# Performance work log

Hardware: AMD Instinct MI355X
Metric: run time of the kernel (lower is better)

Reference implementation:

```python
import jax, jax.numpy as jnp
import numpy as np

L, B, S, D = 12, 2, 2048, 768
QK, H, V = 128, 512, 32000
SCALE = 128 ** (-0.5)


def setup_inputs() -> dict:
    key = jax.random.key(0)
    ks = jax.random.split(key, 11)
    p = lambda k, shp: jax.random.normal(k, shp, dtype=jnp.float32) * 0.02
    return {
        "layer_outputs": jax.random.normal(ks[0], (L, B, S, D), dtype=jnp.float32),
        "Wq": p(ks[1], (D, QK)), "bq": jnp.zeros((QK,), jnp.float32),
        "Wk": p(ks[2], (D, QK)), "bk": jnp.zeros((QK,), jnp.float32),
        "Wv": p(ks[3], (D, H)),  "bv": jnp.zeros((H,), jnp.float32),
        "W1": p(ks[4], (H, H // 2)), "b1": jnp.zeros((H // 2,), jnp.float32),
        "W2": p(ks[5], (H // 2, V)), "b2": jnp.zeros((V,), jnp.float32),
    }


def reference(layer_outputs, Wq, bq, Wk, bk, Wv, bv, W1, b1, W2, b2):
    # layer_outputs: (L, B, S, D) -> h: (S, L, B, D) as in torch permute(2,0,1,3)
    h = jnp.transpose(layer_outputs, (2, 0, 1, 3))
    q_in = h.mean(axis=1)                              # (S, B, D)
    q = jax.nn.relu(q_in @ Wq + bq)                    # (S, B, 128)
    k = jax.nn.relu(h @ Wk + bk)                       # (S, L, B, 128)
    scores = jnp.einsum('sbd,slbd->slb', q, k)[..., None] * SCALE  # (S, L, B, 1)
    attn = jax.nn.softmax(scores, axis=1)              # softmax over layer axis
    v = h @ Wv + bv                                    # (S, L, B, H)
    agg = jnp.sum(attn * v, axis=1)                    # (S, B, H)
    agg = jnp.transpose(agg, (1, 0, 2))                # (B, S, H)
    mid = jax.nn.relu(agg @ W1 + b1)                   # (B, S, H//2); dropout is eval-mode identity
    return mid @ W2 + b2                               # (B, S, V)
```

## Files before the change

kernel.cpp:

```cpp
#include <hip/hip_runtime.h>

#define Snum 2048
#define SCALE 0.08838834764831845f

typedef __attribute__((ext_vector_type(8))) __bf16 bf16x8;
typedef __attribute__((ext_vector_type(4))) float f32x4;

__device__ inline unsigned short f2bf(float f) {
    unsigned int u = __float_as_uint(f);
    unsigned int r = u + 0x7FFFu + ((u >> 16) & 1u);
    return (unsigned short)(r >> 16);
}
__device__ inline float bf2f(unsigned short u) {
    return __uint_as_float(((unsigned)u) << 16);
}
__device__ inline void gld_lds16(const unsigned short* g, unsigned short* l) {
    __builtin_amdgcn_global_load_lds(
        (const __attribute__((address_space(1))) unsigned int*)g,
        (__attribute__((address_space(3))) unsigned int*)l, 16, 0, 0);
}

__global__ __launch_bounds__(256) void prep_weights(
    const float* __restrict__ Wv, unsigned short* __restrict__ Wvbf,
    const float* __restrict__ W1, unsigned short* __restrict__ W1t,
    const float* __restrict__ Wk, const float* __restrict__ Wq,
    unsigned short* __restrict__ Wqkt)
{
    const int id = blockIdx.x;
    if (id < 384) {
        const int base = (id * 256 + threadIdx.x) * 4;
        const float4 v = *(const float4*)(Wv + base);
        ushort4 o;
        o.x = f2bf(v.x); o.y = f2bf(v.y); o.z = f2bf(v.z); o.w = f2bf(v.w);
        *(ushort4*)(Wvbf + base) = o;
        return;
    }
    __shared__ float t[32][33];
    const float* in; unsigned short* out; int K, N, bx, by;
    if (id < 512)      { int q = id - 384; in = W1; out = W1t;  K = 512; N = 256; bx = q & 7; by = q >> 3; }
    else if (id < 608) { int q = id - 512; in = Wk; out = Wqkt; K = 768; N = 128; bx = q & 3; by = q >> 2; }
    else               { int q = id - 608; in = Wq; out = Wqkt + (size_t)128 * 768; K = 768; N = 128; bx = q & 3; by = q >> 2; }

    const int tx = threadIdx.x & 31, ty = threadIdx.x >> 5;
    #pragma unroll
    for (int i = 0; i < 4; ++i) {
        int k = by * 32 + ty + i * 8, n = bx * 32 + tx;
        t[ty + i * 8][tx] = in[(size_t)k * N + n];
    }
    __syncthreads();
    #pragma unroll
    for (int i = 0; i < 4; ++i) {
        int n = bx * 32 + ty + i * 8, k = by * 32 + tx;
        out[(size_t)n * K + k] = f2bf(t[tx][ty + i * 8]);
    }
}

__global__ __launch_bounds__(256) void bias_prime(
    const unsigned short* __restrict__ W1t, const float* __restrict__ bv,
    const float* __restrict__ b1, float* __restrict__ bp)
{
    const int n = threadIdx.x;
    float s = b1[n];
    const unsigned short* row = W1t + (size_t)n * 512;
    for (int h = 0; h < 512; h += 8) {
        uint4 u = *(const uint4*)(row + h);
        const unsigned short* v = (const unsigned short*)&u;
        #pragma unroll
        for (int i = 0; i < 8; ++i) s += bv[h + i] * bf2f(v[i]);
    }
    bp[n] = s;
}

__global__ __launch_bounds__(256) void proj_qk(
    const float* __restrict__ x, const unsigned short* __restrict__ Bt,
    const float* __restrict__ bk,
    unsigned short* __restrict__ Kall,
    unsigned short* __restrict__ Pq)
{
    __shared__ __align__(16) unsigned short As[2][64 * 32];
    __shared__ __align__(16) unsigned short Bs[2][256 * 32];
    const int tid = threadIdx.x;
    const int wid = tid >> 6, lane = tid & 63;
    const int wn = wid * 64;
    const int lr = lane & 15, g = lane >> 4;
    const int r0 = blockIdx.x * 64;
    const int K = 768, NT = 24;

    const int arow = tid >> 2, akc = (tid & 3) * 8;

    f32x4 acc[4][4] = {};

    float4 a0 = *(const float4*)(x + (size_t)(r0 + arow) * K + akc);
    float4 a1 = *(const float4*)(x + (size_t)(r0 + arow) * K + akc + 4);
    {
        unsigned short v[8];
        v[0] = f2bf(a0.x); v[1] = f2bf(a0.y); v[2] = f2bf(a0.z); v[3] = f2bf(a0.w);
        v[4] = f2bf(a1.x); v[5] = f2bf(a1.y); v[6] = f2bf(a1.z); v[7] = f2bf(a1.w);
        *(uint4*)&As[0][arow * 32 + akc] = *(uint4*)v;
    }
    #pragma unroll
    for (int c = 0; c < 4; ++c) {
        const int rr = wid * 64 + c * 16;
        gld_lds16(Bt + (size_t)(rr + (lane >> 2)) * K + (lane & 3) * 8, &Bs[0][rr * 32]);
    }
    __syncthreads();

    for (int t = 0; t < NT; ++t) {
        const int cur = t & 1, nxt = cur ^ 1;
        if (t + 1 < NT) {
            const int k0 = (t + 1) * 32;
            a0 = *(const float4*)(x + (size_t)(r0 + arow) * K + k0 + akc);
            a1 = *(const float4*)(x + (size_t)(r0 + arow) * K + k0 + akc + 4);
            #pragma unroll
            for (int c = 0; c < 4; ++c) {
                const int rr = wid * 64 + c * 16;
                gld_lds16(Bt + (size_t)(rr + (lane >> 2)) * K + k0 + (lane & 3) * 8,
                          &Bs[nxt][rr * 32]);
            }
        }

        bf16x8 aF[4], bF[4];
        #pragma unroll
        for (int mm = 0; mm < 4; ++mm) aF[mm] = *(const bf16x8*)&As[cur][(mm * 16 + lr) * 32 + g * 8];
        #pragma unroll
        for (int nn = 0; nn < 4; ++nn) bF[nn] = *(const bf16x8*)&Bs[cur][(wn + nn * 16 + lr) * 32 + g * 8];
        #pragma unroll
        for (int mm = 0; mm < 4; ++mm)
            #pragma unroll
            for (int nn = 0; nn < 4; ++nn)
                acc[mm][nn] = __builtin_amdgcn_mfma_f32_16x16x32_bf16(bF[nn], aF[mm], acc[mm][nn], 0, 0, 0);

        if (t + 1 < NT) {
            unsigned short v[8];
            v[0] = f2bf(a0.x); v[1] = f2bf(a0.y); v[2] = f2bf(a0.z); v[3] = f2bf(a0.w);
            v[4] = f2bf(a1.x); v[5] = f2bf(a1.y); v[6] = f2bf(a1.z); v[7] = f2bf(a1.w);
            *(uint4*)&As[nxt][arow * 32 + akc] = *(uint4*)v;
        }
        __syncthreads();
    }

    #pragma unroll
    for (int mm = 0; mm < 4; ++mm)
        #pragma unroll
        for (int nn = 0; nn < 4; ++nn) {
            const int row = r0 + mm * 16 + lr;
            const int colb = wn + nn * 16 + g * 4;
            unsigned short o[4];
            if (colb < 128) {
                #pragma unroll
                for (int reg = 0; reg < 4; ++reg) {
                    float kv = acc[mm][nn][reg] + bk[colb + reg];
                    o[reg] = f2bf(kv > 0.f ? kv : 0.f);
                }
                *(ushort4*)&Kall[(size_t)row * 128 + colb] = *(ushort4*)o;
            } else {
                #pragma unroll
                for (int reg = 0; reg < 4; ++reg) o[reg] = f2bf(acc[mm][nn][reg]);
                *(ushort4*)&Pq[(size_t)row * 128 + (colb - 128)] = *(ushort4*)o;
            }
        }
}

__global__ __launch_bounds__(256) void scores_plus_w2t(
    const float* __restrict__ x,
    const unsigned short* __restrict__ Pq,
    const float* __restrict__ bq,
    const unsigned short* __restrict__ Kall,
    unsigned short* __restrict__ hbar,
    const float* __restrict__ W2, unsigned short* __restrict__ W2t)
{
    if (blockIdx.x >= 1024) {
        __shared__ float t[32][33];
        const int id = blockIdx.x - 1024;
        const int bx = id >> 3, by = id & 7;
        const int tx = threadIdx.x & 31, ty = threadIdx.x >> 5;
        #pragma unroll
        for (int i = 0; i < 4; ++i) {
            int k = by * 32 + ty + i * 8, n = bx * 32 + tx;
            t[ty + i * 8][tx] = W2[(size_t)k * 32000 + n];
        }
        __syncthreads();
        #pragma unroll
        for (int i = 0; i < 4; ++i) {
            int n = bx * 32 + ty + i * 8, k = by * 32 + tx;
            W2t[(size_t)n * 256 + k] = f2bf(t[tx][ty + i * 8]);
        }
        return;
    }

    const int wid = threadIdx.x >> 6, lane = threadIdx.x & 63;
    const int r = blockIdx.x * 4 + wid;
    const int b = r >> 11, s = r & 2047;

    float qa = 0.f, qb_ = 0.f;
    #pragma unroll
    for (int l = 0; l < 12; ++l) {
        const unsigned short* prow = Pq + ((size_t)(l * 2 + b) * Snum + s) * 128 + lane * 2;
        unsigned int u = *(const unsigned int*)prow;
        qa += bf2f((unsigned short)(u & 0xFFFF));
        qb_ += bf2f((unsigned short)(u >> 16));
    }
    float q0 = qa * (1.0f / 12.0f) + bq[lane * 2];
    float q1 = qb_ * (1.0f / 12.0f) + bq[lane * 2 + 1];
    q0 = q0 > 0.f ? q0 : 0.f;
    q1 = q1 > 0.f ? q1 : 0.f;
    q0 = bf2f(f2bf(q0)); q1 = bf2f(f2bf(q1));

    float sc[12];
    #pragma unroll
    for (int l = 0; l < 12; ++l) {
        const unsigned short* krow = Kall + ((size_t)(l * 2 + b) * Snum + s) * 128 + lane * 2;
        unsigned int u = *(const unsigned int*)krow;
        float p = q0 * bf2f((unsigned short)(u & 0xFFFF)) + q1 * bf2f((unsigned short)(u >> 16));
        #pragma unroll
        for (int off = 32; off > 0; off >>= 1) p += __shfl_xor(p, off, 64);
        sc[l] = p * SCALE;
    }
    float m = sc[0];
    #pragma unroll
    for (int l = 1; l < 12; ++l) m = fmaxf(m, sc[l]);
    float att[12], den = 0.f;
    #pragma unroll
    for (int l = 0; l < 12; ++l) { att[l] = __expf(sc[l] - m); den += att[l]; }
    const float inv = 1.0f / den;
    #pragma unroll
    for (int l = 0; l < 12; ++l) att[l] *= inv;

    #pragma unroll
    for (int jv = 0; jv < 3; ++jv) {
        const int d0 = jv * 256 + lane * 4;
        float a0 = 0.f, a1 = 0.f, a2 = 0.f, a3 = 0.f;
        #pragma unroll
        for (int l = 0; l < 12; ++l) {
            const float4 v = *(const float4*)(x + ((size_t)(l * 2 + b) * Snum + s) * 768 + d0);
            a0 += att[l] * v.x; a1 += att[l] * v.y; a2 += att[l] * v.z; a3 += att[l] * v.w;
        }
        ushort4 o;
        o.x = f2bf(a0); o.y = f2bf(a1); o.z = f2bf(a2); o.w = f2bf(a3);
        *(ushort4*)(hbar + (size_t)r * 768 + d0) = o;
    }
}

template <int RELU, int OUT_BF16, int BIAS>
__global__ __launch_bounds__(256) void gemm64(
    const unsigned short* __restrict__ A, const unsigned short* __restrict__ Bt,
    const float* __restrict__ bias, void* __restrict__ out, int M, int N, int K)
{
    __shared__ __align__(16) unsigned short As[2][64 * 32];
    __shared__ __align__(16) unsigned short Bs[2][64 * 32];
    const int tid = threadIdx.x;
    const int bn = blockIdx.x, bm = blockIdx.y;
    const int wid = tid >> 6, lane = tid & 63;
    const int wm = (wid >> 1) * 32, wn = (wid & 1) * 32;
    const int lr = lane & 15, g = lane >> 4;
    const int r0 = bm * 64, c0 = bn * 64;
    const int NT = K / 32;

    const int srow = lane >> 2, skc = (lane & 3) * 8;

    f32x4 acc[2][2] = {};

    gld_lds16(A  + (size_t)(r0 + wid * 16 + srow) * K + skc, &As[0][wid * 16 * 32]);
    gld_lds16(Bt + (size_t)(c0 + wid * 16 + srow) * K + skc, &Bs[0][wid * 16 * 32]);
    __syncthreads();

    for (int t = 0; t < NT; ++t) {
        const int cur = t & 1, nxt = cur ^ 1;
        if (t + 1 < NT) {
            const int k0 = (t + 1) * 32;
            gld_lds16(A  + (size_t)(r0 + wid * 16 + srow) * K + k0 + skc, &As[nxt][wid * 16 * 32]);
            gld_lds16(Bt + (size_t)(c0 + wid * 16 + srow) * K + k0 + skc, &Bs[nxt][wid * 16 * 32]);
        }

        bf16x8 aF[2], bF[2];
        #pragma unroll
        for (int mm = 0; mm < 2; ++mm) aF[mm] = *(const bf16x8*)&As[cur][(wm + mm * 16 + lr) * 32 + g * 8];
        #pragma unroll
        for (int nn = 0; nn < 2; ++nn) bF[nn] = *(const bf16x8*)&Bs[cur][(wn + nn * 16 + lr) * 32 + g * 8];
        #pragma unroll
        for (int mm = 0; mm < 2; ++mm)
            #pragma unroll
            for (int nn = 0; nn < 2; ++nn)
                acc[mm][nn] = __builtin_amdgcn_mfma_f32_16x16x32_bf16(bF[nn], aF[mm], acc[mm][nn], 0, 0, 0);
        __syncthreads();
    }

    #pragma unroll
    for (int mm = 0; mm < 2; ++mm)
        #pragma unroll
        for (int nn = 0; nn < 2; ++nn) {
            const int orow = r0 + wm + mm * 16 + lr;
            const int colb = c0 + wn + nn * 16 + g * 4;
            float vr[4];
            #pragma unroll
            for (int reg = 0; reg < 4; ++reg) {
                float v = acc[mm][nn][reg] + (BIAS ? bias[colb + reg] : 0.f);
                vr[reg] = (RELU && v < 0.f) ? 0.f : v;
            }
            if (OUT_BF16) {
                unsigned short o[4];
                #pragma unroll
                for (int reg = 0; reg < 4; ++reg) o[reg] = f2bf(vr[reg]);
                *(ushort4*)&((unsigned short*)out)[(size_t)orow * N + colb] = *(ushort4*)o;
            } else {
                *(float4*)&((float*)out)[(size_t)orow * N + colb] = *(float4*)vr;
            }
        }
}

__global__ __launch_bounds__(256) void gemm_out(
    const unsigned short* __restrict__ A,
    const unsigned short* __restrict__ Bt,
    const float* __restrict__ bias, float* __restrict__ out)
{
    __shared__ __align__(16) unsigned short As[2][128 * 32];
    __shared__ __align__(16) unsigned short Bs[2][128 * 32];
    const int K = 256, N = 32000, NT = 8;
    const int orig = blockIdx.x;
    const int swz = (orig & 7) * 1000 + (orig >> 3);
    const int bn = swz >> 5, bm = swz & 31;
    const int tid = threadIdx.x;
    const int wid = tid >> 6, lane = tid & 63;
    const int wm = (wid >> 1) * 64, wn = (wid & 1) * 64;
    const int lr = lane & 15, g = lane >> 4;
    const int r0 = bm * 128, c0 = bn * 128;

    f32x4 acc[4][4] = {};

    #pragma unroll
    for (int c = 0; c < 2; ++c) {
        const int rr = wid * 32 + c * 16;
        gld_lds16(A  + (size_t)(r0 + rr + (lane >> 2)) * K + (lane & 3) * 8, &As[0][rr * 32]);
        gld_lds16(Bt + (size_t)(c0 + rr + (lane >> 2)) * K + (lane & 3) * 8, &Bs[0][rr * 32]);
    }
    __syncthreads();

    for (int t = 0; t < NT; ++t) {
        const int cur = t & 1, nxt = cur ^ 1;
        if (t + 1 < NT) {
            const int k0 = (t + 1) * 32;
            #pragma unroll
            for (int c = 0; c < 2; ++c) {
                const int rr = wid * 32 + c * 16;
                gld_lds16(A  + (size_t)(r0 + rr + (lane >> 2)) * K + k0 + (lane & 3) * 8, &As[nxt][rr * 32]);
                gld_lds16(Bt + (size_t)(c0 + rr + (lane >> 2)) * K + k0 + (lane & 3) * 8, &Bs[nxt][rr * 32]);
            }
        }

        bf16x8 aF[4], bF[4];
        #pragma unroll
        for (int mm = 0; mm < 4; ++mm) aF[mm] = *(const bf16x8*)&As[cur][(wm + mm * 16 + lr) * 32 + g * 8];
        #pragma unroll
        for (int nn = 0; nn < 4; ++nn) bF[nn] = *(const bf16x8*)&Bs[cur][(wn + nn * 16 + lr) * 32 + g * 8];
        #pragma unroll
        for (int mm = 0; mm < 4; ++mm)
            #pragma unroll
            for (int nn = 0; nn < 4; ++nn)
                acc[mm][nn] = __builtin_amdgcn_mfma_f32_16x16x32_bf16(bF[nn], aF[mm], acc[mm][nn], 0, 0, 0);
        __syncthreads();
    }

    #pragma unroll
    for (int mm = 0; mm < 4; ++mm)
        #pragma unroll
        for (int nn = 0; nn < 4; ++nn) {
            const int row = r0 + wm + mm * 16 + lr;
            const int colb = c0 + wn + nn * 16 + g * 4;
            const float4 b4 = *(const float4*)&bias[colb];
            f32x4 o = acc[mm][nn];
            o[0] += b4.x; o[1] += b4.y; o[2] += b4.z; o[3] += b4.w;
            __builtin_nontemporal_store(o, (f32x4*)&out[(size_t)row * N + colb]);
        }
}

extern "C" void kernel_launch(void* const* d_in, const int* in_sizes, int n_in,
                              void* d_out, int out_size, void* d_ws, size_t ws_size,
                              hipStream_t stream) {
    (void)in_sizes; (void)n_in; (void)out_size; (void)ws_size;

    const float* x  = (const float*)d_in[0];
    const float* Wq = (const float*)d_in[1];
    const float* bq = (const float*)d_in[2];
    const float* Wk = (const float*)d_in[3];
    const float* bk = (const float*)d_in[4];
    const float* Wv = (const float*)d_in[5];
    const float* bv = (const float*)d_in[6];
    const float* W1 = (const float*)d_in[7];
    const float* b1 = (const float*)d_in[8];
    const float* W2 = (const float*)d_in[9];
    const float* b2 = (const float*)d_in[10];

    char* p = (char*)d_ws;
    unsigned short* Wqkt  = (unsigned short*)p; p += (size_t)256 * 768 * 2;
    unsigned short* Wvbf  = (unsigned short*)p; p += (size_t)768 * 512 * 2;
    unsigned short* W1t   = (unsigned short*)p; p += (size_t)256 * 512 * 2;
    unsigned short* Gtb   = (unsigned short*)p; p += (size_t)256 * 768 * 2;
    float*          bprim = (float*)p;          p += (size_t)256 * 4;
    unsigned short* W2t   = (unsigned short*)p; p += (size_t)32000 * 256 * 2;
    unsigned short* Kall  = (unsigned short*)p; p += (size_t)49152 * 128 * 2;
    unsigned short* Pq    = (unsigned short*)p; p += (size_t)49152 * 128 * 2;
    unsigned short* hbar  = (unsigned short*)p; p += (size_t)4096 * 768 * 2;
    unsigned short* midb  = (unsigned short*)p; p += (size_t)4096 * 256 * 2;

    prep_weights<<<dim3(704), dim3(256), 0, stream>>>(Wv, Wvbf, W1, W1t, Wk, Wq, Wqkt);

    bias_prime<<<dim3(1), dim3(256), 0, stream>>>(W1t, bv, b1, bprim);

    gemm64<0, 1, 0><<<dim3(768 / 64, 256 / 64), dim3(256), 0, stream>>>(
        W1t, Wvbf, nullptr, Gtb, 256, 768, 512);

    proj_qk<<<dim3(49152 / 64), dim3(256), 0, stream>>>(x, Wqkt, bk, Kall, Pq);

    scores_plus_w2t<<<dim3(1024 + 8000), dim3(256), 0, stream>>>(
        x, Pq, bq, Kall, hbar, W2, W2t);

    gemm64<1, 1, 1><<<dim3(256 / 64, 4096 / 64), dim3(256), 0, stream>>>(
        hbar, Gtb, bprim, midb, 4096, 256, 768);

    gemm_out<<<dim3(8000), dim3(256), 0, stream>>>(midb, W2t, b2, (float*)d_out);
}
```

Baseline: 286.6 us.

## Use 32x32x16 MFMA in output GEMM and fuse bias-prime with G GEMM

The final vocabulary GEMM switches from 16x16x32 bf16 MFMAs to 32x32x16 MFMAs with 2x2 tiles per wave. This reduces the number of LDS fragment reads and MFMA issues per K step. Separately, the bias_prime kernel and the small W1t·Wv GEMM are merged into one 49-block launch, saving one kernel launch. The new output layout must map correctly to the 32x32 accumulator register ordering.

```diff
diff --git a/kernel.cpp b/kernel.cpp
--- a/kernel.cpp
+++ b/kernel.cpp
@@ -5,6 +5,7 @@
 
 typedef __attribute__((ext_vector_type(8))) __bf16 bf16x8;
 typedef __attribute__((ext_vector_type(4))) float f32x4;
+typedef __attribute__((ext_vector_type(16))) float f32x16;
 
 __device__ inline unsigned short f2bf(float f) {
     unsigned int u = __float_as_uint(f);
@@ -55,20 +56,74 @@
     }
 }
 
-__global__ __launch_bounds__(256) void bias_prime(
-    const unsigned short* __restrict__ W1t, const float* __restrict__ bv,
-    const float* __restrict__ b1, float* __restrict__ bp)
-{
-    const int n = threadIdx.x;
-    float s = b1[n];
-    const unsigned short* row = W1t + (size_t)n * 512;
-    for (int h = 0; h < 512; h += 8) {
-        uint4 u = *(const uint4*)(row + h);
-        const unsigned short* v = (const unsigned short*)&u;
-        #pragma unroll
-        for (int i = 0; i < 8; ++i) s += bv[h + i] * bf2f(v[i]);
-    }
-    bp[n] = s;
+__global__ __launch_bounds__(256) void gt_bias(
+    const unsigned short* __restrict__ W1t,
+    const unsigned short* __restrict__ Wvbf,
+    const float* __restrict__ bv, const float* __restrict__ b1,
+    unsigned short* __restrict__ Gtb,
+    float* __restrict__ bp)
+{
+    if (blockIdx.x == 48) {
+        const int n = threadIdx.x;
+        float s = b1[n];
+        const unsigned short* row = W1t + (size_t)n * 512;
+        for (int h = 0; h < 512; h += 8) {
+            uint4 u = *(const uint4*)(row + h);
+            const unsigned short* v = (const unsigned short*)&u;
+            #pragma unroll
+            for (int i = 0; i < 8; ++i) s += bv[h + i] * bf2f(v[i]);
+        }
+        bp[n] = s;
+        return;
+    }
+    __shared__ __align__(16) unsigned short As[2][64 * 32];
+    __shared__ __align__(16) unsigned short Bs[2][64 * 32];
+    const int tid = threadIdx.x;
+    const int bn = blockIdx.x % 12, bm = blockIdx.x / 12;
+    const int wid = tid >> 6, lane = tid & 63;
+    const int wm = (wid >> 1) * 32, wn = (wid & 1) * 32;
+    const int lr = lane & 15, g = lane >> 4;
+    const int r0 = bm * 64, c0 = bn * 64;
+    const int K = 512, NT = 16, N = 768;
+    const int srow = lane >> 2, skc = (lane & 3) * 8;
+
+    f32x4 acc[2][2] = {};
+
+    gld_lds16(W1t  + (size_t)(r0 + wid * 16 + srow) * K + skc, &As[0][wid * 16 * 32]);
+    gld_lds16(Wvbf + (size_t)(c0 + wid * 16 + srow) * K + skc, &Bs[0][wid * 16 * 32]);
+    __syncthreads();
+
+    for (int t = 0; t < NT; ++t) {
+        const int cur = t & 1, nxt = cur ^ 1;
+        if (t + 1 < NT) {
+            const int k0 = (t + 1) * 32;
+            gld_lds16(W1t  + (size_t)(r0 + wid * 16 + srow) * K + k0 + skc, &As[nxt][wid * 16 * 32]);
+            gld_lds16(Wvbf + (size_t)(c0 + wid * 16 + srow) * K + k0 + skc, &Bs[nxt][wid * 16 * 32]);
+        }
+        bf16x8 aF[2], bF[2];
+        #pragma unroll
+        for (int mm = 0; mm < 2; ++mm) aF[mm] = *(const bf16x8*)&As[cur][(wm + mm * 16 + lr) * 32 + g * 8];
+        #pragma unroll
+        for (int nn = 0; nn < 2; ++nn) bF[nn] = *(const bf16x8*)&Bs[cur][(wn + nn * 16 + lr) * 32 + g * 8];
+        #pragma unroll
+        for (int mm = 0; mm < 2; ++mm)
+            #pragma unroll
+            for (int nn = 0; nn < 2; ++nn)
+                acc[mm][nn] = __builtin_amdgcn_mfma_f32_16x16x32_bf16(bF[nn], aF[mm], acc[mm][nn], 0, 0, 0);
+        __syncthreads();
+    }
+
+    #pragma unroll
+    for (int mm = 0; mm < 2; ++mm)
+        #pragma unroll
+        for (int nn = 0; nn < 2; ++nn) {
+            const int orow = r0 + wm + mm * 16 + lr;
+            const int colb = c0 + wn + nn * 16 + g * 4;
+            unsigned short o[4];
+            #pragma unroll
+            for (int reg = 0; reg < 4; ++reg) o[reg] = f2bf(acc[mm][nn][reg]);
+            *(ushort4*)&Gtb[(size_t)orow * N + colb] = *(ushort4*)o;
+        }
 }
 
 __global__ __launch_bounds__(256) void proj_qk(
@@ -322,10 +377,10 @@
     const int tid = threadIdx.x;
     const int wid = tid >> 6, lane = tid & 63;
     const int wm = (wid >> 1) * 64, wn = (wid & 1) * 64;
-    const int lr = lane & 15, g = lane >> 4;
+    const int l31 = lane & 31, hi = lane >> 5;
     const int r0 = bm * 128, c0 = bn * 128;
 
-    f32x4 acc[4][4] = {};
+    f32x16 acc[2][2] = {};
 
     #pragma unroll
     for (int c = 0; c < 2; ++c) {
@@ -347,29 +402,40 @@
             }
         }
 
-        bf16x8 aF[4], bF[4];
-        #pragma unroll
-        for (int mm = 0; mm < 4; ++mm) aF[mm] = *(const bf16x8*)&As[cur][(wm + mm * 16 + lr) * 32 + g * 8];
-        #pragma unroll
-        for (int nn = 0; nn < 4; ++nn) bF[nn] = *(const bf16x8*)&Bs[cur][(wn + nn * 16 + lr) * 32 + g * 8];
-        #pragma unroll
-        for (int mm = 0; mm < 4; ++mm)
-            #pragma unroll
-            for (int nn = 0; nn < 4; ++nn)
-                acc[mm][nn] = __builtin_amdgcn_mfma_f32_16x16x32_bf16(bF[nn], aF[mm], acc[mm][nn], 0, 0, 0);
+        #pragma unroll
+        for (int ksub = 0; ksub < 2; ++ksub) {
+            bf16x8 aF[2], bF[2];
+            #pragma unroll
+            for (int mm = 0; mm < 2; ++mm)
+                aF[mm] = *(const bf16x8*)&As[cur][(wm + mm * 32 + l31) * 32 + ksub * 16 + hi * 8];
+            #pragma unroll
+            for (int nn = 0; nn < 2; ++nn)
+                bF[nn] = *(const bf16x8*)&Bs[cur][(wn + nn * 32 + l31) * 32 + ksub * 16 + hi * 8];
+            #pragma unroll
+            for (int mm = 0; mm < 2; ++mm)
+                #pragma unroll
+                for (int nn = 0; nn < 2; ++nn)
+                    acc[mm][nn] = __builtin_amdgcn_mfma_f32_32x32x16_bf16(bF[nn], aF[mm], acc[mm][nn], 0, 0, 0);
+        }
         __syncthreads();
     }
 
     #pragma unroll
-    for (int mm = 0; mm < 4; ++mm)
-        #pragma unroll
-        for (int nn = 0; nn < 4; ++nn) {
-            const int row = r0 + wm + mm * 16 + lr;
-            const int colb = c0 + wn + nn * 16 + g * 4;
-            const float4 b4 = *(const float4*)&bias[colb];
-            f32x4 o = acc[mm][nn];
-            o[0] += b4.x; o[1] += b4.y; o[2] += b4.z; o[3] += b4.w;
-            __builtin_nontemporal_store(o, (f32x4*)&out[(size_t)row * N + colb]);
+    for (int mm = 0; mm < 2; ++mm)
+        #pragma unroll
+        for (int nn = 0; nn < 2; ++nn) {
+            const int row = r0 + wm + mm * 32 + l31;
+            #pragma unroll
+            for (int q = 0; q < 4; ++q) {
+                const int colb = c0 + wn + nn * 32 + q * 8 + hi * 4;
+                const float4 b4 = *(const float4*)&bias[colb];
+                f32x4 o;
+                o[0] = acc[mm][nn][q * 4 + 0] + b4.x;
+                o[1] = acc[mm][nn][q * 4 + 1] + b4.y;
+                o[2] = acc[mm][nn][q * 4 + 2] + b4.z;
+                o[3] = acc[mm][nn][q * 4 + 3] + b4.w;
+                __builtin_nontemporal_store(o, (f32x4*)&out[(size_t)row * N + colb]);
+            }
         }
 }
 
@@ -404,10 +470,7 @@
 
     prep_weights<<<dim3(704), dim3(256), 0, stream>>>(Wv, Wvbf, W1, W1t, Wk, Wq, Wqkt);
 
-    bias_prime<<<dim3(1), dim3(256), 0, stream>>>(W1t, bv, b1, bprim);
-
-    gemm64<0, 1, 0><<<dim3(768 / 64, 256 / 64), dim3(256), 0, stream>>>(
-        W1t, Wvbf, nullptr, Gtb, 256, 768, 512);
+    gt_bias<<<dim3(49), dim3(256), 0, stream>>>(W1t, Wvbf, bv, b1, Gtb, bprim);
 
     proj_qk<<<dim3(49152 / 64), dim3(256), 0, stream>>>(x, Wqkt, bk, Kall, Pq);
 
```

Result: slower. 725.6 us (+153.2%).

## Fuse weight prep, bias fold and Wv·W1 product into one kernel

Applied to the files above, without the earlier changes.

Replaces three launches (weight conversion/transposes, single-block bias fold, and a bf16 MFMA GEMM computing Gtb = W1^T·Wv^T) with one kernel. Its blocks either transpose Wq/Wk, compute the folded bias directly from fp32 W1, or compute 8 columns of Gtb with scalar fp32 FMAs from an LDS-staged slice of Wv. This removes two kernel launches and the intermediate bf16 Wv/W1t buffers, at the cost of doing the small 256x768x512 product on scalar ALUs instead of matrix cores. The product is also now accumulated from fp32 inputs rather than bf16-rounded ones.

```diff
diff --git a/kernel.cpp b/kernel.cpp
--- a/kernel.cpp
+++ b/kernel.cpp
@@ -20,55 +20,67 @@
         (__attribute__((address_space(3))) unsigned int*)l, 16, 0, 0);
 }
 
-__global__ __launch_bounds__(256) void prep_weights(
-    const float* __restrict__ Wv, unsigned short* __restrict__ Wvbf,
-    const float* __restrict__ W1, unsigned short* __restrict__ W1t,
+__global__ __launch_bounds__(256) void prep_all(
     const float* __restrict__ Wk, const float* __restrict__ Wq,
-    unsigned short* __restrict__ Wqkt)
+    unsigned short* __restrict__ Wqkt,
+    const float* __restrict__ Wv,
+    const float* __restrict__ W1,
+    const float* __restrict__ bv, const float* __restrict__ b1,
+    unsigned short* __restrict__ Gtb,
+    float* __restrict__ bp)
 {
     const int id = blockIdx.x;
-    if (id < 384) {
-        const int base = (id * 256 + threadIdx.x) * 4;
-        const float4 v = *(const float4*)(Wv + base);
-        ushort4 o;
-        o.x = f2bf(v.x); o.y = f2bf(v.y); o.z = f2bf(v.z); o.w = f2bf(v.w);
-        *(ushort4*)(Wvbf + base) = o;
+    const int tid = threadIdx.x;
+
+    if (id < 192) {
+        __shared__ float t[32][33];
+        const int q = (id < 96) ? id : (id - 96);
+        const float* in = (id < 96) ? Wk : Wq;
+        unsigned short* out = Wqkt + (id < 96 ? 0 : (size_t)128 * 768);
+        const int bx = q & 3, by = q >> 2;
+        const int tx = tid & 31, ty = tid >> 5;
+        #pragma unroll
+        for (int i = 0; i < 4; ++i) {
+            int k = by * 32 + ty + i * 8, n = bx * 32 + tx;
+            t[ty + i * 8][tx] = in[(size_t)k * 128 + n];
+        }
+        __syncthreads();
+        #pragma unroll
+        for (int i = 0; i < 4; ++i) {
+            int n = bx * 32 + ty + i * 8, k = by * 32 + tx;
+            out[(size_t)n * 768 + k] = f2bf(t[tx][ty + i * 8]);
+        }
         return;
     }
-    __shared__ float t[32][33];
-    const float* in; unsigned short* out; int K, N, bx, by;
-    if (id < 512)      { int q = id - 384; in = W1; out = W1t;  K = 512; N = 256; bx = q & 7; by = q >> 3; }
-    else if (id < 608) { int q = id - 512; in = Wk; out = Wqkt; K = 768; N = 128; bx = q & 3; by = q >> 2; }
-    else               { int q = id - 608; in = Wq; out = Wqkt + (size_t)128 * 768; K = 768; N = 128; bx = q & 3; by = q >> 2; }
-
-    const int tx = threadIdx.x & 31, ty = threadIdx.x >> 5;
-    #pragma unroll
-    for (int i = 0; i < 4; ++i) {
-        int k = by * 32 + ty + i * 8, n = bx * 32 + tx;
-        t[ty + i * 8][tx] = in[(size_t)k * N + n];
+
+    if (id == 288) {
+        const int n = tid;
+        float s = b1[n];
+        for (int h = 0; h < 512; ++h) s += bv[h] * W1[(size_t)h * 256 + n];
+        bp[n] = s;
+        return;
+    }
+
+    __shared__ float wv[8][512];
+    const int v0 = (id - 192) * 8;
+    for (int i = tid; i < 8 * 512; i += 256) {
+        const int v = i >> 9, h = i & 511;
+        wv[v][h] = Wv[(size_t)(v0 + v) * 512 + h];
     }
     __syncthreads();
-    #pragma unroll
-    for (int i = 0; i < 4; ++i) {
-        int n = bx * 32 + ty + i * 8, k = by * 32 + tx;
-        out[(size_t)n * K + k] = f2bf(t[tx][ty + i * 8]);
-    }
-}
-
-__global__ __launch_bounds__(256) void bias_prime(
-    const unsigned short* __restrict__ W1t, const float* __restrict__ bv,
-    const float* __restrict__ b1, float* __restrict__ bp)
-{
-    const int n = threadIdx.x;
-    float s = b1[n];
-    const unsigned short* row = W1t + (size_t)n * 512;
-    for (int h = 0; h < 512; h += 8) {
-        uint4 u = *(const uint4*)(row + h);
-        const unsigned short* v = (const unsigned short*)&u;
-        #pragma unroll
-        for (int i = 0; i < 8; ++i) s += bv[h + i] * bf2f(v[i]);
-    }
-    bp[n] = s;
+
+    const int n = tid;
+    float acc[8] = {};
+    for (int h = 0; h < 512; ++h) {
+        const float w1 = W1[(size_t)h * 256 + n];
+        #pragma unroll
+        for (int v = 0; v < 8; ++v) acc[v] += wv[v][h] * w1;
+    }
+    unsigned short o[8];
+    #pragma unroll
+    for (int v = 0; v < 8; ++v) o[v] = f2bf(acc[v]);
+    *(ushort4*)&Gtb[(size_t)n * 768 + v0]     = *(ushort4*)&o[0];
+    *(ushort4*)&Gtb[(size_t)n * 768 + v0 + 4] = *(ushort4*)&o[4];
 }
 
 __global__ __launch_bounds__(256) void proj_qk(
@@ -392,8 +404,6 @@
 
     char* p = (char*)d_ws;
     unsigned short* Wqkt  = (unsigned short*)p; p += (size_t)256 * 768 * 2;
-    unsigned short* Wvbf  = (unsigned short*)p; p += (size_t)768 * 512 * 2;
-    unsigned short* W1t   = (unsigned short*)p; p += (size_t)256 * 512 * 2;
     unsigned short* Gtb   = (unsigned short*)p; p += (size_t)256 * 768 * 2;
     float*          bprim = (float*)p;          p += (size_t)256 * 4;
     unsigned short* W2t   = (unsigned short*)p; p += (size_t)32000 * 256 * 2;
@@ -402,12 +412,7 @@
     unsigned short* hbar  = (unsigned short*)p; p += (size_t)4096 * 768 * 2;
     unsigned short* midb  = (unsigned short*)p; p += (size_t)4096 * 256 * 2;
 
-    prep_weights<<<dim3(704), dim3(256), 0, stream>>>(Wv, Wvbf, W1, W1t, Wk, Wq, Wqkt);
-
-    bias_prime<<<dim3(1), dim3(256), 0, stream>>>(W1t, bv, b1, bprim);
-
-    gemm64<0, 1, 0><<<dim3(768 / 64, 256 / 64), dim3(256), 0, stream>>>(
-        W1t, Wvbf, nullptr, Gtb, 256, 768, 512);
+    prep_all<<<dim3(289), dim3(256), 0, stream>>>(Wk, Wq, Wqkt, Wv, W1, bv, b1, Gtb, bprim);
 
     proj_qk<<<dim3(49152 / 64), dim3(256), 0, stream>>>(x, Wqkt, bk, Kall, Pq);
 
```

New measurement: 284.2 us. Within noise of the previous version (-0.8%).
